# Kernel optimization log

Measured on AMD Instinct MI355X. Metric: run time of the kernel, lower is better.

## Reference

```python
import jax, jax.numpy as jnp
import numpy as np

BATCH, SEQ, DIM = 256, 80, 1024
HEADS = 8
HID = 4 * DIM
EPS = 1e-5


def _ln(x, g, b):
    mu = jnp.mean(x, axis=-1, keepdims=True)
    var = jnp.mean((x - mu) ** 2, axis=-1, keepdims=True)
    return (x - mu) * jax.lax.rsqrt(var + EPS) * g + b


def setup_inputs() -> dict:
    key = jax.random.key(0)
    ks = jax.random.split(key, 8)
    w = lambda k, shape: jax.random.normal(k, shape, dtype=jnp.float32) * 0.02
    return {
        "x": jax.random.normal(ks[0], (BATCH, SEQ, DIM), dtype=jnp.float32),
        "Wq": w(ks[1], (DIM, DIM)),
        "Wk": w(ks[2], (DIM, DIM)),
        "Wv": w(ks[3], (DIM, DIM)),
        "bias_table": w(ks[4], (2 * SEQ - 1, HEADS)),
        "to_out_g": jnp.ones((DIM,), jnp.float32),
        "to_out_b": jnp.zeros((DIM,), jnp.float32),
        "ln1_g": jnp.ones((DIM,), jnp.float32),
        "ln1_b": jnp.zeros((DIM,), jnp.float32),
        "ln2_g": jnp.ones((DIM,), jnp.float32),
        "ln2_b": jnp.zeros((DIM,), jnp.float32),
        "fc1_w": w(ks[5], (DIM, HID)),
        "fc1_b": jnp.zeros((HID,), jnp.float32),
        "fc2_w": w(ks[6], (HID, DIM)),
        "fc2_b": jnp.zeros((DIM,), jnp.float32),
    }


def reference(x, Wq, Wk, Wv, bias_table, to_out_g, to_out_b,
              ln1_g, ln1_b, ln2_g, ln2_b, fc1_w, fc1_b, fc2_w, fc2_b):
    B, S, E = x.shape
    H = HEADS
    D = E // H
    scale = E ** (-0.5)  # NOTE: full emb_size scale, faithful to source

    q = (x @ Wq).reshape(B, S, H, D).transpose(0, 2, 1, 3)  # bhsd
    k = (x @ Wk).reshape(B, S, H, D).transpose(0, 2, 1, 3)
    v = (x @ Wv).reshape(B, S, H, D).transpose(0, 2, 1, 3)

    attn = jnp.einsum('bhqd,bhkd->bhqk', q, k) * scale
    attn = jax.nn.softmax(attn, axis=-1)

    # relative bias added AFTER softmax (non-standard, faithful)
    idx = jnp.arange(S)[:, None] - jnp.arange(S)[None, :] + (S - 1)  # [S,S] in [0,2S-2]
    bias = bias_table[idx].transpose(2, 0, 1)  # (H, S, S)
    attn = attn + bias[None]

    out = jnp.einsum('bhqk,bhkd->bhqd', attn, v)
    out = out.transpose(0, 2, 1, 3).reshape(B, S, E)
    out = _ln(out, to_out_g, to_out_b)  # LayerNorm inside attention (to_out)

    x = _ln(x + out, ln1_g, ln1_b)      # post-norm residual 1
    h = jax.nn.gelu(x @ fc1_w + fc1_b, approximate=False)  # torch nn.GELU exact
    ff = h @ fc2_w + fc2_b
    return _ln(x + ff, ln2_g, ln2_b)    # post-norm residual 2
```

## Files before the change

kernel.cpp:

```cpp
#include <hip/hip_runtime.h>
#include <stdint.h>

#define BATCH 256
#define SEQ   80
#define DIM   1024
#define HEADS 8
#define HDIM  128
#define HID   4096
#define NTOK  (BATCH * SEQ)

typedef unsigned short u16;
using short8_t = __attribute__((ext_vector_type(8))) short;
using f32x4    = __attribute__((ext_vector_type(4))) float;

__device__ __forceinline__ u16 f2bf(float f) {
  unsigned u = __float_as_uint(f);
  u += 0x7fffu + ((u >> 16) & 1u);
  return (u16)(u >> 16);
}
__device__ __forceinline__ float bf2f(u16 u) {
  return __uint_as_float(((unsigned)u) << 16);
}

__device__ __forceinline__ float gelu_exact(float v) {
  return 0.5f * v * (1.0f + erff(v * 0.70710678118654752f));
}

#define GLD16(gp, lp)                                                   \
  __builtin_amdgcn_global_load_lds(                                     \
      (__attribute__((address_space(1))) void*)(void*)(gp),             \
      (__attribute__((address_space(3))) void*)(void*)(lp), 16, 0, 0)

__global__ __launch_bounds__(256) void cast_bf16_kernel(
    const float* __restrict__ in, u16* __restrict__ out, int n4) {
  int i = blockIdx.x * 256 + threadIdx.x;
  int stride = gridDim.x * 256;
  for (; i < n4; i += stride) {
    float4 v = ((const float4*)in)[i];
    uint2 o;
    o.x = (unsigned)f2bf(v.x) | ((unsigned)f2bf(v.y) << 16);
    o.y = (unsigned)f2bf(v.z) | ((unsigned)f2bf(v.w) << 16);
    ((uint2*)out)[i] = o;
  }
}

__global__ __launch_bounds__(256) void transpose_cast_kernel(
    const float* __restrict__ in, u16* __restrict__ out, int R, int C) {
  __shared__ float tile[32][33];
  int c0 = blockIdx.x * 32, r0 = blockIdx.y * 32;
  for (int k = 0; k < 4; k++) {
    int i = threadIdx.y + k * 8;
    tile[i][threadIdx.x] = in[(size_t)(r0 + i) * C + c0 + threadIdx.x];
  }
  __syncthreads();
  for (int k = 0; k < 4; k++) {
    int i = threadIdx.y + k * 8;
    out[(size_t)(c0 + i) * R + r0 + threadIdx.x] = f2bf(tile[threadIdx.x][i]);
  }
}

template <int EPI>
__global__ __launch_bounds__(512, 2) void gemm8p(
    const u16* __restrict__ A, const u16* __restrict__ Bt,
    const float* __restrict__ bias, u16* __restrict__ outp,
    int M, int N, int K, int ntn) {
  __shared__ __align__(16) u16 lds[65536];

  const int tid = threadIdx.x;
  const int lane = tid & 63, wave = tid >> 6;
  const int wm = wave >> 2, wn = wave & 3;
  const int lo = lane & 15, hi = lane >> 4;

  const int nwg = gridDim.x;
  int q8 = nwg >> 3, r8 = nwg & 7;
  int xcd = blockIdx.x & 7, off = blockIdx.x >> 3;
  int swz = (xcd < r8 ? xcd * (q8 + 1) : r8 * (q8 + 1) + (xcd - r8) * q8) + off;
  const int bn = swz % ntn, bm = swz / ntn;
  const size_t arow0 = (size_t)bm * 256, bcol0 = (size_t)bn * 256;

  const int srow = tid >> 2;
  const int slb  = (tid & 3) ^ ((srow >> 1) & 3);
  const u16* sA = A + (arow0 + srow) * K + slb * 8;
  const u16* sB = Bt + (bcol0 + srow) * K + slb * 8;
  const size_t sstep = 128 * (size_t)K;

  const int arow = wm * 128 + lo;
  const int brow = wn * 64 + lo;
  const int aoff = arow * 32 + (hi ^ ((arow >> 1) & 3)) * 8;
  const int boff = brow * 32 + (hi ^ ((brow >> 1) & 3)) * 8;

  f32x4 acc[8][4] = {};
  const int NT = K >> 6;
  const int NI = NT >> 1;

#define STG(mat, buf, kh, t)                                                  \
  do {                                                                        \
    const u16* s_ = ((mat) ? sB : sA) + (size_t)(t) * 64 + (kh) * 32;         \
    u16* d_ = lds + ((((buf) << 2) | ((mat) << 1) | (kh)) << 13) + wave * 512;\
    GLD16(s_, d_);                                                            \
    GLD16(s_ + sstep, d_ + 4096);                                             \
  } while (0)

#define RD_A(buf, kh, mh, dst)                                                \
  _Pragma("unroll") for (int mi = 0; mi < 4; ++mi)                            \
      dst[mi] = *(const short8_t*)&lds[((((buf) << 2) | (kh)) << 13) + aoff + \
                                       ((mh) * 4 + mi) * 512];

#define RD_B(buf, kh, dst)                                                    \
  _Pragma("unroll") for (int ni = 0; ni < 4; ++ni)                            \
      dst[ni] = *(const short8_t*)&lds[((((buf) << 2) | 2 | (kh)) << 13) +    \
                                       boff + ni * 512];

#define MFMA16(mh, a_, b_)                                                    \
  __builtin_amdgcn_s_setprio(1);                                              \
  _Pragma("unroll") for (int mi = 0; mi < 4; ++mi)                            \
  _Pragma("unroll") for (int ni = 0; ni < 4; ++ni)                            \
      acc[(mh) * 4 + mi][ni] = __builtin_amdgcn_mfma_f32_16x16x32_bf16(       \
          a_[mi], b_[ni], acc[(mh) * 4 + mi][ni], 0, 0, 0);                   \
  __builtin_amdgcn_s_setprio(0);

#define BAR()   asm volatile("s_barrier" ::: "memory")
#define LGKM0() asm volatile("s_waitcnt lgkmcnt(0)" ::: "memory")
#define VM(n)   asm volatile("s_waitcnt vmcnt(" #n ")" ::: "memory")

  STG(0, 0, 0, 0); STG(1, 0, 0, 0); STG(0, 0, 1, 0); STG(1, 0, 1, 0);
  STG(0, 1, 0, 1); STG(1, 1, 0, 1); STG(1, 1, 1, 1);
  asm volatile("s_waitcnt vmcnt(0)" ::: "memory");
  BAR();

  short8_t aR0[4], aR1[4], bR0[4], bR1[4];

  for (int i = 0; i < NI - 1; ++i) {
    const int t0 = 2 * i, t1 = 2 * i + 1;
    RD_A(0, 0, 0, aR0); RD_B(0, 0, bR0);
    LGKM0(); MFMA16(0, aR0, bR0);
    RD_A(0, 0, 1, aR1);
    STG(0, 1, 1, t1);
    VM(8); BAR();
    LGKM0(); MFMA16(1, aR1, bR0);
    RD_A(0, 1, 0, aR0); RD_B(0, 1, bR1);
    STG(1, 0, 0, t0 + 2);
    BAR();
    LGKM0(); MFMA16(0, aR0, bR1);
    RD_A(0, 1, 1, aR1);
    STG(0, 0, 0, t0 + 2);
    VM(8); BAR();
    LGKM0(); MFMA16(1, aR1, bR1);
    RD_A(1, 0, 0, aR0); RD_B(1, 0, bR0);
    STG(1, 0, 1, t0 + 2);
    BAR();
    LGKM0(); MFMA16(0, aR0, bR0);
    RD_A(1, 0, 1, aR1);
    STG(0, 0, 1, t0 + 2);
    VM(8); BAR();
    LGKM0(); MFMA16(1, aR1, bR0);
    RD_A(1, 1, 0, aR0); RD_B(1, 1, bR1);
    STG(1, 1, 0, t1 + 2);
    BAR();
    LGKM0(); MFMA16(0, aR0, bR1);
    RD_A(1, 1, 1, aR1);
    STG(0, 1, 0, t1 + 2);
    BAR();
    LGKM0(); MFMA16(1, aR1, bR1);
    STG(1, 1, 1, t1 + 2);
    VM(10); BAR();
  }

  {
    const int t1 = NT - 1;
    RD_A(0, 0, 0, aR0); RD_B(0, 0, bR0);
    LGKM0(); MFMA16(0, aR0, bR0);
    RD_A(0, 0, 1, aR1);
    STG(0, 1, 1, t1);
    VM(8); BAR();
    LGKM0(); MFMA16(1, aR1, bR0);
    RD_A(0, 1, 0, aR0); RD_B(0, 1, bR1);
    BAR();
    LGKM0(); MFMA16(0, aR0, bR1);
    RD_A(0, 1, 1, aR1);
    VM(4); BAR();
    LGKM0(); MFMA16(1, aR1, bR1);
    RD_A(1, 0, 0, aR0); RD_B(1, 0, bR0);
    BAR();
    LGKM0(); MFMA16(0, aR0, bR0);
    RD_A(1, 0, 1, aR1);
    VM(0); BAR();
    LGKM0(); MFMA16(1, aR1, bR0);
    RD_A(1, 1, 0, aR0); RD_B(1, 1, bR1);
    BAR();
    LGKM0(); MFMA16(0, aR0, bR1);
    RD_A(1, 1, 1, aR1);
    BAR();
    LGKM0(); MFMA16(1, aR1, bR1);
    BAR();
  }
#undef STG
#undef RD_A
#undef RD_B
#undef MFMA16

  asm volatile("s_waitcnt vmcnt(0)" ::: "memory");
  __syncthreads();

  u16* ct = lds;
#pragma unroll
  for (int n = 0; n < 4; ++n) {
    int col = wn * 64 + n * 16 + lo;
    float bv = 0.f;
    if constexpr (EPI != 0) bv = bias[bcol0 + col];
#pragma unroll
    for (int m = 0; m < 8; ++m) {
#pragma unroll
      for (int j = 0; j < 4; ++j) {
        int row = wm * 128 + m * 16 + hi * 4 + j;
        float v = acc[m][n][j] + bv;
        if constexpr (EPI == 1) v = gelu_exact(v);
        ct[row * 256 + col] = f2bf(v);
      }
    }
  }
  __syncthreads();
  u16* op = outp + arow0 * (size_t)N + bcol0;
#pragma unroll
  for (int i = 0; i < 16; ++i) {
    int c = i * 512 + tid;
    int row = c >> 5, o2 = (c & 31) * 8;
    *(short8_t*)(op + (size_t)row * N + o2) = *(const short8_t*)&ct[row * 256 + o2];
  }
}

__global__ __launch_bounds__(64) void attn_kernel(
    const u16* __restrict__ QKV, const float* __restrict__ bias_table,
    u16* __restrict__ attnout) {
  __shared__ __align__(16) u16 Kt[80 * 128];
  __shared__ __align__(16) u16 Vt[96 * 128];
  __shared__ float bias_l[159];

  const int bh = blockIdx.x;
  const int b = bh >> 3, h = bh & 7;
  const int lane = threadIdx.x, lo = lane & 15, hi = lane >> 4;
  const size_t tokbase = (size_t)b * SEQ * 3072;
  const u16* Qg = QKV + tokbase + h * HDIM;
  const u16* Kg = QKV + tokbase + 1024 + h * HDIM;
  const u16* Vg = QKV + tokbase + 2048 + h * HDIM;

#pragma unroll
  for (int i = 0; i < 20; i++) {
    int flat = i * 64 + lane;
    int row = flat >> 4;
    int col = (flat & 15) * 8;
    GLD16(Kg + (size_t)row * 3072 + col, &Kt[i * 512]);
    GLD16(Vg + (size_t)row * 3072 + col, &Vt[i * 512]);
  }
  for (int i = lane; i < 16 * 128; i += 64) Vt[80 * 128 + i] = 0;
  for (int i = lane; i < 159; i += 64) bias_l[i] = bias_table[i * 8 + h];
  asm volatile("s_waitcnt vmcnt(0)" ::: "memory");
  __syncthreads();

  f32x4 sa[5][5] = {};
#pragma unroll
  for (int ks = 0; ks < 4; ks++) {
    short8_t ak[5], bq[5];
#pragma unroll
    for (int m = 0; m < 5; m++)
      ak[m] = *(const short8_t*)&Kt[(m * 16 + lo) * 128 + ks * 32 + hi * 8];
#pragma unroll
    for (int n = 0; n < 5; n++)
      bq[n] = *(const short8_t*)(Qg + (size_t)(n * 16 + lo) * 3072 + ks * 32 + hi * 8);
#pragma unroll
    for (int m = 0; m < 5; m++)
#pragma unroll
      for (int n = 0; n < 5; n++)
        sa[m][n] = __builtin_amdgcn_mfma_f32_16x16x32_bf16(ak[m], bq[n], sa[m][n], 0, 0, 0);
  }
  __syncthreads();

  u16* p_lds = Kt;
  for (int i = lane; i < 80 * 16; i += 64) {
    int q = i >> 4, c = 80 + (i & 15);
    p_lds[q * 104 + c] = 0;
  }
  const float scale = 0.03125f;
#pragma unroll
  for (int n = 0; n < 5; n++) {
    float mx = -1e30f;
#pragma unroll
    for (int m = 0; m < 5; m++)
#pragma unroll
      for (int j = 0; j < 4; j++) {
        sa[m][n][j] *= scale;
        mx = fmaxf(mx, sa[m][n][j]);
      }
    mx = fmaxf(mx, __shfl_xor(mx, 16));
    mx = fmaxf(mx, __shfl_xor(mx, 32));
    float sm = 0.f;
#pragma unroll
    for (int m = 0; m < 5; m++)
#pragma unroll
      for (int j = 0; j < 4; j++) {
        float e = __expf(sa[m][n][j] - mx);
        sa[m][n][j] = e;
        sm += e;
      }
    sm += __shfl_xor(sm, 16);
    sm += __shfl_xor(sm, 32);
    float inv = 1.0f / sm;
    int q = n * 16 + lo;
#pragma unroll
    for (int m = 0; m < 5; m++)
#pragma unroll
      for (int j = 0; j < 4; j++) {
        int key = m * 16 + hi * 4 + j;
        float pv = sa[m][n][j] * inv + bias_l[q - key + 79];
        p_lds[q * 104 + key] = f2bf(pv);
      }
  }
  __syncthreads();

#pragma unroll
  for (int half = 0; half < 2; half++) {
    f32x4 oa[5][4] = {};
#pragma unroll
    for (int ks = 0; ks < 3; ks++) {
      short8_t ap[5];
#pragma unroll
      for (int m = 0; m < 5; m++)
        ap[m] = *(const short8_t*)&p_lds[(m * 16 + lo) * 104 + ks * 32 + hi * 8];
      short8_t bv[4];
#pragma unroll
      for (int nd = 0; nd < 4; nd++) {
        int d = (half * 4 + nd) * 16 + lo;
        short8_t tt;
#pragma unroll
        for (int j = 0; j < 8; j++)
          tt[j] = (short)Vt[(ks * 32 + hi * 8 + j) * 128 + d];
        bv[nd] = tt;
      }
#pragma unroll
      for (int m = 0; m < 5; m++)
#pragma unroll
        for (int nd = 0; nd < 4; nd++)
          oa[m][nd] = __builtin_amdgcn_mfma_f32_16x16x32_bf16(ap[m], bv[nd], oa[m][nd], 0, 0, 0);
    }
#pragma unroll
    for (int m = 0; m < 5; m++)
#pragma unroll
      for (int nd = 0; nd < 4; nd++)
#pragma unroll
        for (int j = 0; j < 4; j++) {
          int q = m * 16 + hi * 4 + j;
          int d = (half * 4 + nd) * 16 + lo;
          attnout[((size_t)b * SEQ + q) * DIM + h * HDIM + d] = f2bf(oa[m][nd][j]);
        }
  }
}

__device__ __forceinline__ void block_reduce2(float& a, float& b, float* sbuf) {
#pragma unroll
  for (int m = 1; m < 64; m <<= 1) {
    a += __shfl_xor(a, m);
    b += __shfl_xor(b, m);
  }
  int w = threadIdx.x >> 6;
  if ((threadIdx.x & 63) == 0) { sbuf[w * 2] = a; sbuf[w * 2 + 1] = b; }
  __syncthreads();
  a = sbuf[0] + sbuf[2] + sbuf[4] + sbuf[6];
  b = sbuf[1] + sbuf[3] + sbuf[5] + sbuf[7];
  __syncthreads();
}

__global__ __launch_bounds__(256) void fuse1_kernel(
    const u16* __restrict__ attnout, const float* __restrict__ x,
    const float* __restrict__ og, const float* __restrict__ ob,
    const float* __restrict__ g1, const float* __restrict__ b1,
    u16* __restrict__ x1b) {
  __shared__ float sbuf[8];
  const size_t base = (size_t)blockIdx.x * DIM;
  float a[4], r[4];
  float s0 = 0.f, s1 = 0.f;
#pragma unroll
  for (int i = 0; i < 4; i++) {
    int idx = threadIdx.x + i * 256;
    a[i] = bf2f(attnout[base + idx]);
    s0 += a[i];
    s1 += a[i] * a[i];
  }
  block_reduce2(s0, s1, sbuf);
  float mu = s0 * (1.f / DIM);
  float rstd = rsqrtf(s1 * (1.f / DIM) - mu * mu + 1e-5f);
  float t0 = 0.f, t1 = 0.f;
#pragma unroll
  for (int i = 0; i < 4; i++) {
    int idx = threadIdx.x + i * 256;
    float o = (a[i] - mu) * rstd * og[idx] + ob[idx];
    r[i] = x[base + idx] + o;
    t0 += r[i];
    t1 += r[i] * r[i];
  }
  block_reduce2(t0, t1, sbuf);
  float mu2 = t0 * (1.f / DIM);
  float rstd2 = rsqrtf(t1 * (1.f / DIM) - mu2 * mu2 + 1e-5f);
#pragma unroll
  for (int i = 0; i < 4; i++) {
    int idx = threadIdx.x + i * 256;
    x1b[base + idx] = f2bf((r[i] - mu2) * rstd2 * g1[idx] + b1[idx]);
  }
}

__global__ __launch_bounds__(256) void fuse2_kernel(
    const u16* __restrict__ x1b, const u16* __restrict__ ff,
    const float* __restrict__ g2, const float* __restrict__ b2,
    float* __restrict__ out) {
  __shared__ float sbuf[8];
  const size_t base = (size_t)blockIdx.x * DIM;
  float r[4];
  float s0 = 0.f, s1 = 0.f;
#pragma unroll
  for (int i = 0; i < 4; i++) {
    int idx = threadIdx.x + i * 256;
    r[i] = bf2f(x1b[base + idx]) + bf2f(ff[base + idx]);
    s0 += r[i];
    s1 += r[i] * r[i];
  }
  block_reduce2(s0, s1, sbuf);
  float mu = s0 * (1.f / DIM);
  float rstd = rsqrtf(s1 * (1.f / DIM) - mu * mu + 1e-5f);
#pragma unroll
  for (int i = 0; i < 4; i++) {
    int idx = threadIdx.x + i * 256;
    out[base + idx] = (r[i] - mu) * rstd * g2[idx] + b2[idx];
  }
}

extern "C" void kernel_launch(void* const* d_in, const int* in_sizes, int n_in,
                              void* d_out, int out_size, void* d_ws, size_t ws_size,
                              hipStream_t stream) {
  const float* x        = (const float*)d_in[0];
  const float* Wq       = (const float*)d_in[1];
  const float* Wk       = (const float*)d_in[2];
  const float* Wv       = (const float*)d_in[3];
  const float* bias_tab = (const float*)d_in[4];
  const float* og       = (const float*)d_in[5];
  const float* ob       = (const float*)d_in[6];
  const float* g1       = (const float*)d_in[7];
  const float* b1       = (const float*)d_in[8];
  const float* g2       = (const float*)d_in[9];
  const float* b2       = (const float*)d_in[10];
  const float* fc1w     = (const float*)d_in[11];
  const float* fc1b     = (const float*)d_in[12];
  const float* fc2w     = (const float*)d_in[13];
  const float* fc2b     = (const float*)d_in[14];

  char* ws = (char*)d_ws;
  u16* wqkvT = (u16*)(ws + 0);
  u16* fc1T  = (u16*)(ws + 6291456ull);
  u16* fc2T  = (u16*)(ws + 14680064ull);
  u16* pbuf  = (u16*)(ws + 23068672ull);
  u16* qbuf  = (u16*)(ws + 65011712ull);
  char* cbuf = ws + 106954752ull;
  size_t cavail = ws_size > 106954752ull ? ws_size - 106954752ull : 0;

  int cb = 1;
  while (cb < 16 && (size_t)(BATCH / cb) * SEQ * 3072 * 2 > cavail) cb <<= 1;
  int cf = 1;
  while (cf < 16 && (size_t)(NTOK / cf) * HID * 2 > cavail) cf <<= 1;

  dim3 tb(32, 8);
  cast_bf16_kernel<<<2048, 256, 0, stream>>>(x, qbuf, NTOK * DIM / 4);
  transpose_cast_kernel<<<dim3(32, 32), tb, 0, stream>>>(Wq, wqkvT, 1024, 1024);
  transpose_cast_kernel<<<dim3(32, 32), tb, 0, stream>>>(Wk, wqkvT + 1024 * 1024, 1024, 1024);
  transpose_cast_kernel<<<dim3(32, 32), tb, 0, stream>>>(Wv, wqkvT + 2 * 1024 * 1024, 1024, 1024);
  transpose_cast_kernel<<<dim3(128, 32), tb, 0, stream>>>(fc1w, fc1T, 1024, 4096);
  transpose_cast_kernel<<<dim3(32, 128), tb, 0, stream>>>(fc2w, fc2T, 4096, 1024);

  {
    const int nb = BATCH / cb;
    const int rows = nb * SEQ;
    u16* qkvc = (u16*)cbuf;
    const int nwg = (rows / 256) * (3072 / 256);
    for (int c = 0; c < cb; ++c) {
      const u16* xb_c = qbuf + (size_t)c * rows * DIM;
      gemm8p<0><<<nwg, 512, 0, stream>>>(xb_c, wqkvT, nullptr, qkvc,
                                         rows, 3072, 1024, 3072 / 256);
      attn_kernel<<<nb * HEADS, 64, 0, stream>>>(
          qkvc, bias_tab, pbuf + (size_t)c * rows * DIM);
    }
  }

  fuse1_kernel<<<NTOK, 256, 0, stream>>>(pbuf, x, og, ob, g1, b1, qbuf);

  {
    const int rows = NTOK / cf;
    u16* hc = (u16*)cbuf;
    const int nwg1 = (rows / 256) * (HID / 256);
    const int nwg2 = (rows / 256) * (DIM / 256);
    for (int c = 0; c < cf; ++c) {
      gemm8p<1><<<nwg1, 512, 0, stream>>>(qbuf + (size_t)c * rows * DIM, fc1T,
                                          fc1b, hc, rows, HID, 1024, HID / 256);
      gemm8p<2><<<nwg2, 512, 0, stream>>>(hc, fc2T, fc2b,
                                          pbuf + (size_t)c * rows * DIM,
                                          rows, 1024, HID, DIM / 256);
    }
  }

  fuse2_kernel<<<NTOK, 256, 0, stream>>>(qbuf, pbuf, g2, b2, (float*)d_out);
}
```

Before: 759.5 us.

## Split-K the fc2 GEMM and fold partial sums into final LayerNorm

Generalizes the GEMM kernel to process a K-slice per workgroup and write to one of two output buffers, launching fc2 with two K-splits to double the workgroup count. The two bf16 partials plus the fc2 bias are summed inside the final residual LayerNorm kernel, which now runs per chunk. It also drops explicit lgkmcnt(0) waits before MFMA blocks, relying on compiler-inserted waits. This adds an extra partial-output write/read and bf16 rounding of each partial.

```diff
diff --git a/kernel.cpp b/kernel.cpp
--- a/kernel.cpp
+++ b/kernel.cpp
@@ -60,10 +60,10 @@
 }
 
 template <int EPI>
-__global__ __launch_bounds__(512, 2) void gemm8p(
+__global__ __launch_bounds__(512, 2) void gemm8s(
     const u16* __restrict__ A, const u16* __restrict__ Bt,
-    const float* __restrict__ bias, u16* __restrict__ outp,
-    int M, int N, int K, int ntn) {
+    const float* __restrict__ bias, u16* __restrict__ outp, u16* __restrict__ outp1,
+    int M, int N, int Keff, int Ks, int ntn, int ntm) {
   __shared__ __align__(16) u16 lds[65536];
 
   const int tid = threadIdx.x;
@@ -75,14 +75,17 @@
   int q8 = nwg >> 3, r8 = nwg & 7;
   int xcd = blockIdx.x & 7, off = blockIdx.x >> 3;
   int swz = (xcd < r8 ? xcd * (q8 + 1) : r8 * (q8 + 1) + (xcd - r8) * q8) + off;
-  const int bn = swz % ntn, bm = swz / ntn;
+  const int per = ntn * ntm;
+  const int kp = swz / per, rem = swz % per;
+  const int bn = rem % ntn, bm = rem / ntn;
   const size_t arow0 = (size_t)bm * 256, bcol0 = (size_t)bn * 256;
+  const int kbase = kp * Keff;
 
   const int srow = tid >> 2;
   const int slb  = (tid & 3) ^ ((srow >> 1) & 3);
-  const u16* sA = A + (arow0 + srow) * K + slb * 8;
-  const u16* sB = Bt + (bcol0 + srow) * K + slb * 8;
-  const size_t sstep = 128 * (size_t)K;
+  const u16* sA = A + (arow0 + srow) * (size_t)Ks + kbase + slb * 8;
+  const u16* sB = Bt + (bcol0 + srow) * (size_t)Ks + kbase + slb * 8;
+  const size_t sstep = 128 * (size_t)Ks;
 
   const int arow = wm * 128 + lo;
   const int brow = wn * 64 + lo;
@@ -90,7 +93,7 @@
   const int boff = brow * 32 + (hi ^ ((brow >> 1) & 3)) * 8;
 
   f32x4 acc[8][4] = {};
-  const int NT = K >> 6;
+  const int NT = Keff >> 6;
   const int NI = NT >> 1;
 
 #define STG(mat, buf, kh, t)                                                  \
@@ -120,7 +123,6 @@
   __builtin_amdgcn_s_setprio(0);
 
 #define BAR()   asm volatile("s_barrier" ::: "memory")
-#define LGKM0() asm volatile("s_waitcnt lgkmcnt(0)" ::: "memory")
 #define VM(n)   asm volatile("s_waitcnt vmcnt(" #n ")" ::: "memory")
 
   STG(0, 0, 0, 0); STG(1, 0, 0, 0); STG(0, 0, 1, 0); STG(1, 0, 1, 0);
@@ -133,35 +135,35 @@
   for (int i = 0; i < NI - 1; ++i) {
     const int t0 = 2 * i, t1 = 2 * i + 1;
     RD_A(0, 0, 0, aR0); RD_B(0, 0, bR0);
-    LGKM0(); MFMA16(0, aR0, bR0);
+    MFMA16(0, aR0, bR0);
     RD_A(0, 0, 1, aR1);
     STG(0, 1, 1, t1);
     VM(8); BAR();
-    LGKM0(); MFMA16(1, aR1, bR0);
+    MFMA16(1, aR1, bR0);
     RD_A(0, 1, 0, aR0); RD_B(0, 1, bR1);
     STG(1, 0, 0, t0 + 2);
     BAR();
-    LGKM0(); MFMA16(0, aR0, bR1);
+    MFMA16(0, aR0, bR1);
     RD_A(0, 1, 1, aR1);
     STG(0, 0, 0, t0 + 2);
     VM(8); BAR();
-    LGKM0(); MFMA16(1, aR1, bR1);
+    MFMA16(1, aR1, bR1);
     RD_A(1, 0, 0, aR0); RD_B(1, 0, bR0);
     STG(1, 0, 1, t0 + 2);
     BAR();
-    LGKM0(); MFMA16(0, aR0, bR0);
+    MFMA16(0, aR0, bR0);
     RD_A(1, 0, 1, aR1);
     STG(0, 0, 1, t0 + 2);
     VM(8); BAR();
-    LGKM0(); MFMA16(1, aR1, bR0);
+    MFMA16(1, aR1, bR0);
     RD_A(1, 1, 0, aR0); RD_B(1, 1, bR1);
     STG(1, 1, 0, t1 + 2);
     BAR();
-    LGKM0(); MFMA16(0, aR0, bR1);
+    MFMA16(0, aR0, bR1);
     RD_A(1, 1, 1, aR1);
     STG(0, 1, 0, t1 + 2);
     BAR();
-    LGKM0(); MFMA16(1, aR1, bR1);
+    MFMA16(1, aR1, bR1);
     STG(1, 1, 1, t1 + 2);
     VM(10); BAR();
   }
@@ -169,29 +171,29 @@
   {
     const int t1 = NT - 1;
     RD_A(0, 0, 0, aR0); RD_B(0, 0, bR0);
-    LGKM0(); MFMA16(0, aR0, bR0);
+    MFMA16(0, aR0, bR0);
     RD_A(0, 0, 1, aR1);
     STG(0, 1, 1, t1);
     VM(8); BAR();
-    LGKM0(); MFMA16(1, aR1, bR0);
+    MFMA16(1, aR1, bR0);
     RD_A(0, 1, 0, aR0); RD_B(0, 1, bR1);
     BAR();
-    LGKM0(); MFMA16(0, aR0, bR1);
+    MFMA16(0, aR0, bR1);
     RD_A(0, 1, 1, aR1);
     VM(4); BAR();
-    LGKM0(); MFMA16(1, aR1, bR1);
+    MFMA16(1, aR1, bR1);
     RD_A(1, 0, 0, aR0); RD_B(1, 0, bR0);
     BAR();
-    LGKM0(); MFMA16(0, aR0, bR0);
+    MFMA16(0, aR0, bR0);
     RD_A(1, 0, 1, aR1);
     VM(0); BAR();
-    LGKM0(); MFMA16(1, aR1, bR0);
+    MFMA16(1, aR1, bR0);
     RD_A(1, 1, 0, aR0); RD_B(1, 1, bR1);
     BAR();
-    LGKM0(); MFMA16(0, aR0, bR1);
+    MFMA16(0, aR0, bR1);
     RD_A(1, 1, 1, aR1);
     BAR();
-    LGKM0(); MFMA16(1, aR1, bR1);
+    MFMA16(1, aR1, bR1);
     BAR();
   }
 #undef STG
@@ -220,7 +222,7 @@
     }
   }
   __syncthreads();
-  u16* op = outp + arow0 * (size_t)N + bcol0;
+  u16* op = (kp ? outp1 : outp) + arow0 * (size_t)N + bcol0;
 #pragma unroll
   for (int i = 0; i < 16; ++i) {
     int c = i * 512 + tid;
@@ -408,7 +410,8 @@
 }
 
 __global__ __launch_bounds__(256) void fuse2_kernel(
-    const u16* __restrict__ x1b, const u16* __restrict__ ff,
+    const u16* __restrict__ x1b, const u16* __restrict__ p0,
+    const u16* __restrict__ p1, const float* __restrict__ fc2b,
     const float* __restrict__ g2, const float* __restrict__ b2,
     float* __restrict__ out) {
   __shared__ float sbuf[8];
@@ -418,7 +421,8 @@
 #pragma unroll
   for (int i = 0; i < 4; i++) {
     int idx = threadIdx.x + i * 256;
-    r[i] = bf2f(x1b[base + idx]) + bf2f(ff[base + idx]);
+    r[i] = bf2f(x1b[base + idx]) + bf2f(p0[base + idx]) + bf2f(p1[base + idx]) +
+           fc2b[idx];
     s0 += r[i];
     s1 += r[i] * r[i];
   }
@@ -463,7 +467,7 @@
   int cb = 1;
   while (cb < 16 && (size_t)(BATCH / cb) * SEQ * 3072 * 2 > cavail) cb <<= 1;
   int cf = 1;
-  while (cf < 16 && (size_t)(NTOK / cf) * HID * 2 > cavail) cf <<= 1;
+  while (cf < 16 && (size_t)(NTOK / cf) * (HID + DIM) * 2 > cavail) cf <<= 1;
 
   dim3 tb(32, 8);
   cast_bf16_kernel<<<2048, 256, 0, stream>>>(x, qbuf, NTOK * DIM / 4);
@@ -477,11 +481,12 @@
     const int nb = BATCH / cb;
     const int rows = nb * SEQ;
     u16* qkvc = (u16*)cbuf;
-    const int nwg = (rows / 256) * (3072 / 256);
+    const int ntm = rows / 256;
+    const int nwg = ntm * 12;
     for (int c = 0; c < cb; ++c) {
       const u16* xb_c = qbuf + (size_t)c * rows * DIM;
-      gemm8p<0><<<nwg, 512, 0, stream>>>(xb_c, wqkvT, nullptr, qkvc,
-                                         rows, 3072, 1024, 3072 / 256);
+      gemm8s<0><<<nwg, 512, 0, stream>>>(xb_c, wqkvT, nullptr, qkvc, qkvc,
+                                         rows, 3072, 1024, 1024, 12, ntm);
       attn_kernel<<<nb * HEADS, 64, 0, stream>>>(
           qkvc, bias_tab, pbuf + (size_t)c * rows * DIM);
     }
@@ -491,17 +496,18 @@
 
   {
     const int rows = NTOK / cf;
-    u16* hc = (u16*)cbuf;
-    const int nwg1 = (rows / 256) * (HID / 256);
-    const int nwg2 = (rows / 256) * (DIM / 256);
+    u16* hc  = (u16*)cbuf;
+    u16* p1c = (u16*)(cbuf + (size_t)rows * HID * 2);
+    const int ntm = rows / 256;
     for (int c = 0; c < cf; ++c) {
-      gemm8p<1><<<nwg1, 512, 0, stream>>>(qbuf + (size_t)c * rows * DIM, fc1T,
-                                          fc1b, hc, rows, HID, 1024, HID / 256);
-      gemm8p<2><<<nwg2, 512, 0, stream>>>(hc, fc2T, fc2b,
-                                          pbuf + (size_t)c * rows * DIM,
-                                          rows, 1024, HID, DIM / 256);
+      const size_t off = (size_t)c * rows * DIM;
+      gemm8s<1><<<ntm * 16, 512, 0, stream>>>(qbuf + off, fc1T, fc1b, hc, hc,
+                                              rows, HID, 1024, 1024, 16, ntm);
+      gemm8s<0><<<ntm * 4 * 2, 512, 0, stream>>>(hc, fc2T, nullptr,
+                                                 pbuf + off, p1c,
+                                                 rows, 1024, 2048, 4096, 4, ntm);
+      fuse2_kernel<<<rows, 256, 0, stream>>>(qbuf + off, pbuf + off, p1c, fc2b,
+                                             g2, b2, (float*)d_out + off);
     }
   }
-
-  fuse2_kernel<<<NTOK, 256, 0, stream>>>(qbuf, pbuf, g2, b2, (float*)d_out);
-}
+}
```

After: 747.7 us (median of 2 runs). About the same (-1.6%).
